# Kernel tuning notes

Measured on AMD Instinct MI355X. Metric: run time of the kernel, lower is better.

Reference implementation:

```python
import jax, jax.numpy as jnp
import numpy as np

B, N, DIM, H = 4, 2048, 1024, 16
HEAD_DIM = DIM // H
SCALE = HEAD_DIM ** (-0.5)


def setup_inputs() -> dict:
    key = jax.random.key(0)
    k1, k2, k3 = jax.random.split(key, 3)
    x = jax.random.normal(k1, (B, N, DIM), dtype=jnp.float32)
    # nn.Linear(dim, 3*dim, bias=False): weight shape [3*dim, dim], y = x @ W.T
    w_qkv = jax.random.normal(k2, (3 * DIM, DIM), dtype=jnp.float32) * 0.02
    w_proj = jax.random.normal(k3, (DIM, DIM), dtype=jnp.float32) * 0.02
    return {"x": x, "w_qkv": w_qkv, "w_proj": w_proj}


def reference(x, w_qkv, w_proj):
    Bv, Nv, C = x.shape
    Dh = C // H
    # qkv projection -> [B, N, 3, H, Dh]
    qkv = (x @ w_qkv.T).reshape(Bv, Nv, 3, H, Dh)
    q, k, v = qkv[:, :, 0], qkv[:, :, 1], qkv[:, :, 2]  # each [B, N, H, Dh]
    # scaled dot-product attention per head (online-softmax loop collapses to this)
    scores = jnp.einsum("bnhd,bmhd->bhnm", q, k) * SCALE  # [B, H, N, N]
    attn = jax.nn.softmax(scores, axis=-1)
    out = jnp.einsum("bhnm,bmhd->bnhd", attn, v).reshape(Bv, Nv, C)
    return out @ w_proj.T
```

## Files before the change

kernel.cpp:

```cpp
#include <hip/hip_runtime.h>

typedef __bf16 bf16;
typedef bf16 bf16x8 __attribute__((ext_vector_type(8)));
typedef float f32x4 __attribute__((ext_vector_type(4)));
typedef float f32x16 __attribute__((ext_vector_type(16)));

#define B_   4
#define N_   2048
#define DIM_ 1024
#define H_   16
#define DH_  64
#define M_   (B_ * N_)

#define CEXP 0.18033688f

#define GLOBAL_CP(g) (const __attribute__((address_space(1))) void*)(g)
#define LDS_CP(l)    (__attribute__((address_space(3))) void*)(l)

__global__ __launch_bounds__(256) void cvt_all(
    const float* __restrict__ x, const float* __restrict__ wq,
    const float* __restrict__ wp, bf16* __restrict__ o,
    int nx4, int nwq4, int nwp4)
{
    const int i = blockIdx.x * blockDim.x + threadIdx.x;
    const float* src; int si;
    if (i < nx4)                { src = x;  si = i; }
    else if (i < nx4 + nwq4)    { src = wq; si = i - nx4; }
    else                        { src = wp; si = i - nx4 - nwq4; }
    const float4 v = ((const float4*)src)[si];
    union { bf16 h[4]; uint2 u; } r;
    r.h[0] = (bf16)v.x; r.h[1] = (bf16)v.y;
    r.h[2] = (bf16)v.z; r.h[3] = (bf16)v.w;
    ((uint2*)o)[i] = r.u;
}

__global__ __launch_bounds__(256) void gemm_bt(
    const bf16* __restrict__ A, const bf16* __restrict__ Bm,
    int Ndim, int K, int mode,
    float* __restrict__ outf,
    bf16* __restrict__ qb, bf16* __restrict__ kbv, bf16* __restrict__ vbT)
{
    __shared__ bf16 As[128 * 32];
    __shared__ bf16 Bs[128 * 32];

    const int tid  = threadIdx.x;
    const int wave = tid >> 6;
    const int lane = tid & 63;
    const int quad = lane >> 4;
    const int lr   = lane & 15;
    const int wr   = wave >> 1, wc = wave & 1;
    const int m0 = blockIdx.y * 128;
    const int n0 = blockIdx.x * 128;

    f32x4 acc[4][4];
#pragma unroll
    for (int i = 0; i < 4; i++)
#pragma unroll
        for (int j = 0; j < 4; j++) acc[i][j] = f32x4{0.f, 0.f, 0.f, 0.f};

    const int srow = lane >> 2;
    const int scol = ((lane & 3) ^ ((srow >> 1) & 3)) * 8;

    for (int k0 = 0; k0 < K; k0 += 32) {
        __syncthreads();
#pragma unroll
        for (int j = 0; j < 2; j++) {
            const int rbase = j * 64 + wave * 16;
            __builtin_amdgcn_global_load_lds(
                GLOBAL_CP(A + (size_t)(m0 + rbase + srow) * K + k0 + scol),
                LDS_CP(&As[rbase * 32 + lane * 8]), 16, 0, 0);
            __builtin_amdgcn_global_load_lds(
                GLOBAL_CP(Bm + (size_t)(n0 + rbase + srow) * K + k0 + scol),
                LDS_CP(&Bs[rbase * 32 + lane * 8]), 16, 0, 0);
        }
        __syncthreads();

        bf16x8 af[4], bfr[4];
#pragma unroll
        for (int i = 0; i < 4; i++) {
            const int R = wr * 64 + i * 16 + lr;
            af[i] = *(const bf16x8*)(&As[R * 32 + ((quad ^ ((R >> 1) & 3)) << 3)]);
        }
#pragma unroll
        for (int j = 0; j < 4; j++) {
            const int R = wc * 64 + j * 16 + lr;
            bfr[j] = *(const bf16x8*)(&Bs[R * 32 + ((quad ^ ((R >> 1) & 3)) << 3)]);
        }
#pragma unroll
        for (int i = 0; i < 4; i++)
#pragma unroll
            for (int j = 0; j < 4; j++)
                acc[i][j] = __builtin_amdgcn_mfma_f32_16x16x32_bf16(
                    af[i], bfr[j], acc[i][j], 0, 0, 0);
    }

#pragma unroll
    for (int i = 0; i < 4; i++) {
        const int mbase = m0 + wr * 64 + i * 16 + quad * 4;
#pragma unroll
        for (int j = 0; j < 4; j++) {
            const int n = n0 + wc * 64 + j * 16 + lr;
            if (mode == 0) {
#pragma unroll
                for (int r = 0; r < 4; r++)
                    outf[(size_t)(mbase + r) * Ndim + n] = acc[i][j][r];
            } else {
                const int which = n >> 10;
                const int h = (n >> 6) & 15;
                const int d = n & 63;
                const int b  = mbase >> 11;
                const int t0 = mbase & 2047;
                if (which == 2) {
                    union { uint2 u; bf16 hh[4]; } p;
#pragma unroll
                    for (int r = 0; r < 4; r++) p.hh[r] = (bf16)acc[i][j][r];
                    *(uint2*)(&vbT[(((size_t)(b * 16 + h)) * 64 + d) * 2048 + t0]) = p.u;
                } else {
                    bf16* dst = (which == 0) ? qb : kbv;
                    const float sc = (which == 0) ? CEXP : 1.0f;
#pragma unroll
                    for (int r = 0; r < 4; r++)
                        dst[(((size_t)(b * 16 + h)) * 2048 + t0 + r) * 64 + d] =
                            (bf16)(acc[i][j][r] * sc);
                }
            }
        }
    }
}

__global__ __launch_bounds__(256, 3) void attn_kernel(
    const bf16* __restrict__ qb, const bf16* __restrict__ kb,
    const bf16* __restrict__ vbT, bf16* __restrict__ ao)
{
    __shared__ bf16 Ks[128 * 64];
    __shared__ bf16 Vs[64 * 128];

    const int tid  = threadIdx.x;
    const int wave = tid >> 6;
    const int lane = tid & 63;
    const int l31  = lane & 31;
    const int hh   = lane >> 5;

    const int bid = blockIdx.x;
    const int qt  = (bid >> 3) & 15;
    const int bh  = ((bid >> 7) << 3) | (bid & 7);

    const bf16* Q  = qb  + (size_t)bh * N_ * DH_;
    const bf16* Kp = kb  + (size_t)bh * N_ * DH_;
    const bf16* Vp = vbT + (size_t)bh * DH_ * N_;

    bf16x8 qf[4];
#pragma unroll
    for (int ks = 0; ks < 4; ks++)
        qf[ks] = *(const bf16x8*)(Q + (size_t)(qt * 128 + wave * 32 + l31) * DH_
                                    + ks * 16 + hh * 8);

    const int krow0 = (lane >> 3);
    const int kscol = ((lane & 7) ^ ((lane >> 3) & 7)) * 8;
    const int vrow0 = (lane >> 4);

    float lrow = 0.f;
    f32x16 oacc[2];
#pragma unroll
    for (int d = 0; d < 2; d++)
#pragma unroll
        for (int r = 0; r < 16; r++) oacc[d][r] = 0.f;

    for (int t = 0; t < N_ / 128; t++) {
        __syncthreads();
#pragma unroll
        for (int c = 0; c < 4; c++) {
            const int ii = wave * 4 + c;
            const int krow = ii * 8 + krow0;
            __builtin_amdgcn_global_load_lds(
                GLOBAL_CP(Kp + (size_t)(t * 128 + krow) * DH_ + kscol),
                LDS_CP(&Ks[ii * 512 + lane * 8]), 16, 0, 0);
            const int vrow = ii * 4 + vrow0;
            const int vscol = ((lane & 15) ^ (vrow & 15)) * 8;
            __builtin_amdgcn_global_load_lds(
                GLOBAL_CP(Vp + (size_t)vrow * N_ + t * 128 + vscol),
                LDS_CP(&Vs[ii * 512 + lane * 8]), 16, 0, 0);
        }
        __syncthreads();

        float ssum = 0.f;
#pragma unroll
        for (int kbk = 0; kbk < 4; kbk++) {
            f32x16 e;
#pragma unroll
            for (int r = 0; r < 16; r++) e[r] = 0.f;
#pragma unroll
            for (int ks = 0; ks < 4; ks++) {
                const int R  = kbk * 32 + l31;
                const int ch = ks * 2 + hh;
                bf16x8 ak = *(const bf16x8*)(&Ks[R * 64 + ((ch ^ (R & 7)) << 3)]);
                e = __builtin_amdgcn_mfma_f32_32x32x16_bf16(ak, qf[ks], e, 0, 0, 0);
            }

#pragma unroll
            for (int r = 0; r < 16; r++) {
                e[r] = exp2f(e[r]);
                ssum += e[r];
            }

            float t1[4], t2[4];
#pragma unroll
            for (int j = 0; j < 4; j++) {
                const float s1 = hh ? e[j]     : e[4 + j];
                const float s2 = hh ? e[8 + j] : e[12 + j];
                t1[j] = __shfl_xor(s1, 32);
                t2[j] = __shfl_xor(s2, 32);
            }
            bf16x8 p0, p1;
#pragma unroll
            for (int j = 0; j < 4; j++) {
                p0[j]     = (bf16)(hh ? t1[j]      : e[j]);
                p0[4 + j] = (bf16)(hh ? e[4 + j]   : t1[j]);
                p1[j]     = (bf16)(hh ? t2[j]      : e[8 + j]);
                p1[4 + j] = (bf16)(hh ? e[12 + j]  : t2[j]);
            }

#pragma unroll
            for (int dblk = 0; dblk < 2; dblk++) {
                const int R   = dblk * 32 + l31;
                const int ch0 = kbk * 4 + hh;
                const int ch1 = kbk * 4 + 2 + hh;
                bf16x8 bv0 = *(const bf16x8*)(&Vs[R * 128 + ((ch0 ^ (R & 15)) << 3)]);
                bf16x8 bv1 = *(const bf16x8*)(&Vs[R * 128 + ((ch1 ^ (R & 15)) << 3)]);
                oacc[dblk] = __builtin_amdgcn_mfma_f32_32x32x16_bf16(p0, bv0, oacc[dblk], 0, 0, 0);
                oacc[dblk] = __builtin_amdgcn_mfma_f32_32x32x16_bf16(p1, bv1, oacc[dblk], 0, 0, 0);
            }
        }
        ssum += __shfl_xor(ssum, 32);
        lrow += ssum;
    }

    const int head = bh & 15;
    const int b    = bh >> 4;
    const float linv = 1.0f / lrow;
#pragma unroll
    for (int r = 0; r < 16; r++) {
        const int qr  = (r & 3) + 8 * (r >> 2) + 4 * hh;
        const float inv = __shfl(linv, qr);
        const int qrow = qt * 128 + wave * 32 + qr;
#pragma unroll
        for (int dblk = 0; dblk < 2; dblk++)
            ao[((size_t)(b * 2048 + qrow)) * 1024 + head * 64 + dblk * 32 + l31] =
                (bf16)(oacc[dblk][r] * inv);
    }
}

extern "C" void kernel_launch(void* const* d_in, const int* in_sizes, int n_in,
                              void* d_out, int out_size, void* d_ws, size_t ws_size,
                              hipStream_t stream)
{
    const float* x     = (const float*)d_in[0];
    const float* wqkv  = (const float*)d_in[1];
    const float* wproj = (const float*)d_in[2];
    float* out = (float*)d_out;

    const size_t nx  = (size_t)M_ * DIM_;
    const size_t nwq = (size_t)3 * DIM_ * DIM_;
    const size_t nwp = (size_t)DIM_ * DIM_;
    const size_t seg = (size_t)B_ * H_ * N_ * DH_;

    bf16* xb     = (bf16*)d_ws;
    bf16* wqkvb  = xb + nx;
    bf16* wprojb = wqkvb + nwq;
    bf16* qb     = wprojb + nwp;
    bf16* kb     = qb + seg;
    bf16* vbT    = kb + seg;
    bf16* ao     = xb;

    const int nx4  = (int)(nx / 4), nwq4 = (int)(nwq / 4), nwp4 = (int)(nwp / 4);
    cvt_all<<<(nx4 + nwq4 + nwp4) / 256, 256, 0, stream>>>(
        x, wqkv, wproj, xb, nx4, nwq4, nwp4);

    gemm_bt<<<dim3(24, 64), 256, 0, stream>>>(xb, wqkvb, 3 * DIM_, DIM_, 1,
                                              nullptr, qb, kb, vbT);
    attn_kernel<<<dim3(1024), 256, 0, stream>>>(qb, kb, vbT, ao);
    gemm_bt<<<dim3(8, 64), 256, 0, stream>>>(ao, wprojb, DIM_, DIM_, 0,
                                             out, nullptr, nullptr, nullptr);
}
```

Measured before the change: 311.6 us.

## Double GEMM K-tile to 64 and compute softmax row sums with MFMA

The GEMM kernel now stages 64-wide K slices in LDS with an 8-way XOR swizzle and runs two MFMA sub-steps per load, which halves the number of barrier pairs per K loop. In attention, the row-sum of exponentials is computed by an extra MFMA of the bf16 probabilities against a ones vector, replacing the scalar adds and the cross-lane shuffles. This costs two extra MFMAs per block and 16 more accumulator registers, and the sum is now taken over bf16-rounded probabilities, which matches the numerator exactly.

```diff
diff --git a/kernel.cpp b/kernel.cpp
--- a/kernel.cpp
+++ b/kernel.cpp
@@ -40,8 +40,8 @@
     float* __restrict__ outf,
     bf16* __restrict__ qb, bf16* __restrict__ kbv, bf16* __restrict__ vbT)
 {
-    __shared__ bf16 As[128 * 32];
-    __shared__ bf16 Bs[128 * 32];
+    __shared__ bf16 As[128 * 64];
+    __shared__ bf16 Bs[128 * 64];
 
     const int tid  = threadIdx.x;
     const int wave = tid >> 6;
@@ -58,40 +58,44 @@
 #pragma unroll
         for (int j = 0; j < 4; j++) acc[i][j] = f32x4{0.f, 0.f, 0.f, 0.f};
 
-    const int srow = lane >> 2;
-    const int scol = ((lane & 3) ^ ((srow >> 1) & 3)) * 8;
-
-    for (int k0 = 0; k0 < K; k0 += 32) {
-        __syncthreads();
-#pragma unroll
-        for (int j = 0; j < 2; j++) {
-            const int rbase = j * 64 + wave * 16;
-            __builtin_amdgcn_global_load_lds(
-                GLOBAL_CP(A + (size_t)(m0 + rbase + srow) * K + k0 + scol),
-                LDS_CP(&As[rbase * 32 + lane * 8]), 16, 0, 0);
-            __builtin_amdgcn_global_load_lds(
-                GLOBAL_CP(Bm + (size_t)(n0 + rbase + srow) * K + k0 + scol),
-                LDS_CP(&Bs[rbase * 32 + lane * 8]), 16, 0, 0);
-        }
-        __syncthreads();
-
-        bf16x8 af[4], bfr[4];
-#pragma unroll
-        for (int i = 0; i < 4; i++) {
-            const int R = wr * 64 + i * 16 + lr;
-            af[i] = *(const bf16x8*)(&As[R * 32 + ((quad ^ ((R >> 1) & 3)) << 3)]);
-        }
-#pragma unroll
-        for (int j = 0; j < 4; j++) {
-            const int R = wc * 64 + j * 16 + lr;
-            bfr[j] = *(const bf16x8*)(&Bs[R * 32 + ((quad ^ ((R >> 1) & 3)) << 3)]);
-        }
-#pragma unroll
-        for (int i = 0; i < 4; i++)
-#pragma unroll
-            for (int j = 0; j < 4; j++)
-                acc[i][j] = __builtin_amdgcn_mfma_f32_16x16x32_bf16(
-                    af[i], bfr[j], acc[i][j], 0, 0, 0);
+    const int sl8 = lane >> 3;
+    const int sc8 = ((lane & 7) ^ (sl8 & 7)) * 8;
+
+    for (int k0 = 0; k0 < K; k0 += 64) {
+        __syncthreads();
+#pragma unroll
+        for (int c = 0; c < 4; c++) {
+            const int ii  = wave * 4 + c;
+            const int row = ii * 8 + sl8;
+            __builtin_amdgcn_global_load_lds(
+                GLOBAL_CP(A + (size_t)(m0 + row) * K + k0 + sc8),
+                LDS_CP(&As[ii * 512 + lane * 8]), 16, 0, 0);
+            __builtin_amdgcn_global_load_lds(
+                GLOBAL_CP(Bm + (size_t)(n0 + row) * K + k0 + sc8),
+                LDS_CP(&Bs[ii * 512 + lane * 8]), 16, 0, 0);
+        }
+        __syncthreads();
+
+#pragma unroll
+        for (int s = 0; s < 2; s++) {
+            bf16x8 af[4], bfr[4];
+#pragma unroll
+            for (int i = 0; i < 4; i++) {
+                const int R = wr * 64 + i * 16 + lr;
+                af[i] = *(const bf16x8*)(&As[R * 64 + (((s * 4 + quad) ^ (R & 7)) << 3)]);
+            }
+#pragma unroll
+            for (int j = 0; j < 4; j++) {
+                const int R = wc * 64 + j * 16 + lr;
+                bfr[j] = *(const bf16x8*)(&Bs[R * 64 + (((s * 4 + quad) ^ (R & 7)) << 3)]);
+            }
+#pragma unroll
+            for (int i = 0; i < 4; i++)
+#pragma unroll
+                for (int j = 0; j < 4; j++)
+                    acc[i][j] = __builtin_amdgcn_mfma_f32_16x16x32_bf16(
+                        af[i], bfr[j], acc[i][j], 0, 0, 0);
+        }
     }
 
 #pragma unroll
@@ -155,16 +159,21 @@
         qf[ks] = *(const bf16x8*)(Q + (size_t)(qt * 128 + wave * 32 + l31) * DH_
                                     + ks * 16 + hh * 8);
 
+    bf16x8 onesf;
+#pragma unroll
+    for (int j = 0; j < 8; j++) onesf[j] = (bf16)1.0f;
+
     const int krow0 = (lane >> 3);
     const int kscol = ((lane & 7) ^ ((lane >> 3) & 7)) * 8;
     const int vrow0 = (lane >> 4);
 
-    float lrow = 0.f;
-    f32x16 oacc[2];
+    f32x16 oacc[2], lacc;
 #pragma unroll
     for (int d = 0; d < 2; d++)
 #pragma unroll
         for (int r = 0; r < 16; r++) oacc[d][r] = 0.f;
+#pragma unroll
+    for (int r = 0; r < 16; r++) lacc[r] = 0.f;
 
     for (int t = 0; t < N_ / 128; t++) {
         __syncthreads();
@@ -183,7 +192,6 @@
         }
         __syncthreads();
 
-        float ssum = 0.f;
 #pragma unroll
         for (int kbk = 0; kbk < 4; kbk++) {
             f32x16 e;
@@ -198,10 +206,8 @@
             }
 
 #pragma unroll
-            for (int r = 0; r < 16; r++) {
+            for (int r = 0; r < 16; r++)
                 e[r] = exp2f(e[r]);
-                ssum += e[r];
-            }
 
             float t1[4], t2[4];
 #pragma unroll
@@ -219,6 +225,9 @@
                 p1[j]     = (bf16)(hh ? t2[j]      : e[8 + j]);
                 p1[4 + j] = (bf16)(hh ? e[12 + j]  : t2[j]);
             }
+
+            lacc = __builtin_amdgcn_mfma_f32_32x32x16_bf16(p0, onesf, lacc, 0, 0, 0);
+            lacc = __builtin_amdgcn_mfma_f32_32x32x16_bf16(p1, onesf, lacc, 0, 0, 0);
 
 #pragma unroll
             for (int dblk = 0; dblk < 2; dblk++) {
@@ -231,17 +240,14 @@
                 oacc[dblk] = __builtin_amdgcn_mfma_f32_32x32x16_bf16(p1, bv1, oacc[dblk], 0, 0, 0);
             }
         }
-        ssum += __shfl_xor(ssum, 32);
-        lrow += ssum;
     }
 
     const int head = bh & 15;
     const int b    = bh >> 4;
-    const float linv = 1.0f / lrow;
 #pragma unroll
     for (int r = 0; r < 16; r++) {
         const int qr  = (r & 3) + 8 * (r >> 2) + 4 * hh;
-        const float inv = __shfl(linv, qr);
+        const float inv = 1.0f / lacc[r];
         const int qrow = qt * 128 + wave * 32 + qr;
 #pragma unroll
         for (int dblk = 0; dblk < 2; dblk++)
```

Result: faster. 305.1 us (-2.1%).
